# Kernel optimization log

Measured on AMD Instinct MI355X. Metric: run time of the kernel, lower is better.

## Reference

```python
import jax, jax.numpy as jnp
import numpy as np

B, H, S, D = 4, 16, 4096, 64

def _phi(x):
    # feature map for linear attention: elu(x) + 1 (positive features)
    return jax.nn.elu(x) + 1.0

def setup_inputs() -> dict:
    key = jax.random.key(0)
    kq, kk, kv = jax.random.split(key, 3)
    return {
        "query": jax.random.normal(kq, (B, H, S, D), dtype=jnp.float32),
        "key": jax.random.normal(kk, (B, H, S, D), dtype=jnp.float32),
        "value": jax.random.normal(kv, (B, H, S, D), dtype=jnp.float32),
        "attention_mask": jnp.ones((B, S), dtype=jnp.float32),
    }

def reference(query, key, value, attention_mask):
    head_dim = query.shape[-1]
    scale = 1.0 / jnp.sqrt(jnp.sqrt(jnp.float32(head_dim)))
    q = query * scale
    k = key * scale
    phi_q = _phi(q)
    phi_k = _phi(k)
    m = attention_mask[:, None, :, None]  # [B,1,S,1]
    phi_q = phi_q * m
    phi_k = phi_k * m
    # kv_term: [B,H,D,Dv]
    kv_term = jnp.einsum("bhsd,bhse->bhde", phi_k, value)
    out = jnp.einsum("bhsd,bhde->bhse", phi_q, kv_term)
    # normalizer: phi_q @ sum_s phi_k -> [B,H,S,1]
    k_one = jnp.sum(phi_k, axis=-2)  # [B,H,D]
    normalizer = jnp.einsum("bhsd,bhd->bhs", phi_q, k_one)[..., None]
    return out / (normalizer + 1e-8)
```

## Files before the change

### kernel.cpp

```cpp
#include <hip/hip_runtime.h>

#define BDIM 4
#define HDIM 16
#define SDIM 4096
#define DDIM 64
#define NBH (BDIM * HDIM)

#define NC 16
#define BH_STRIDE (DDIM * DDIM + DDIM)
#define CHUNK_FLOATS (NBH * BH_STRIDE)

__device__ __forceinline__ float phi_f(float x) {
    return x > 0.0f ? x + 1.0f : __expf(x);
}

template<bool ATOMIC>
__global__ __launch_bounds__(256, 2) void la_phase1(
    const float* __restrict__ K, const float* __restrict__ V,
    const float* __restrict__ mask, float* __restrict__ outp, int chunk_rows)
{
    __shared__ __align__(16) float smem[8320];

    const int bh = blockIdx.y;
    const int b  = bh / HDIM;
    const int t  = threadIdx.x;
    const int w  = t >> 6;
    const int l  = t & 63;
    const int rowq = l >> 4;
    const int c4   = (l & 15) << 2;
    const int d0   = (l >> 3) << 3;
    const int e0   = (l & 7) << 3;

    float* kT = smem + w * 1024;

    const float* Kb = K + (size_t)bh * SDIM * DDIM;
    const float* Vb = V + (size_t)bh * SDIM * DDIM;
    const float* mb = mask + (size_t)b * SDIM;
    const float scale = 0.35355339059327373f;

    const int rows_per_wave = chunk_rows >> 2;
    const int s_wave = blockIdx.x * chunk_rows + w * rows_per_wave;
    const int ntiles = rows_per_wave >> 4;

    float acc[8][8] = {};
    float k1s[4] = {0.f, 0.f, 0.f, 0.f};

    float4 kr[4]; float mmr[4];
    #pragma unroll
    for (int j = 0; j < 4; ++j) {
        const int s = s_wave + rowq + (j << 2);
        kr[j]  = *(const float4*)(Kb + (size_t)s * DDIM + c4);
        mmr[j] = mb[s];
    }

    for (int tt = 0; tt < ntiles; ++tt) {
        #pragma unroll
        for (int j = 0; j < 4; ++j) {
            float4 p;
            p.x = phi_f(kr[j].x * scale) * mmr[j];
            p.y = phi_f(kr[j].y * scale) * mmr[j];
            p.z = phi_f(kr[j].z * scale) * mmr[j];
            p.w = phi_f(kr[j].w * scale) * mmr[j];
            k1s[0] += p.x; k1s[1] += p.y; k1s[2] += p.z; k1s[3] += p.w;
            *(float4*)&kT[(rowq + (j << 2)) * DDIM + c4] = p;
        }
        if (tt + 1 < ntiles) {
            #pragma unroll
            for (int j = 0; j < 4; ++j) {
                const int s = s_wave + ((tt + 1) << 4) + rowq + (j << 2);
                kr[j]  = *(const float4*)(Kb + (size_t)s * DDIM + c4);
                mmr[j] = mb[s];
            }
        }

        const int s_tile = s_wave + (tt << 4);
        #pragma unroll
        for (int ss = 0; ss < 16; ++ss) {
            const float4 a0 = *(const float4*)&kT[ss * DDIM + d0];
            const float4 a1 = *(const float4*)&kT[ss * DDIM + d0 + 4];
            const float4 v0 = *(const float4*)(Vb + (size_t)(s_tile + ss) * DDIM + e0);
            const float4 v1 = *(const float4*)(Vb + (size_t)(s_tile + ss) * DDIM + e0 + 4);
            const float av[8] = {a0.x, a0.y, a0.z, a0.w, a1.x, a1.y, a1.z, a1.w};
            const float vv[8] = {v0.x, v0.y, v0.z, v0.w, v1.x, v1.y, v1.z, v1.w};
            #pragma unroll
            for (int i = 0; i < 8; ++i)
                #pragma unroll
                for (int j = 0; j < 8; ++j)
                    acc[i][j] += av[i] * vv[j];
        }
    }

    #pragma unroll
    for (int i = 0; i < 4; ++i) {
        k1s[i] += __shfl_xor(k1s[i], 16);
        k1s[i] += __shfl_xor(k1s[i], 32);
    }

    __syncthreads();
    float* bufA = smem;
    float* bufB = smem + 4160;
    if (w < 2) {
        float* Bp = w ? bufB : bufA;
        #pragma unroll
        for (int i = 0; i < 8; ++i) {
            *(float4*)&Bp[(d0 + i) * DDIM + e0]     = make_float4(acc[i][0], acc[i][1], acc[i][2], acc[i][3]);
            *(float4*)&Bp[(d0 + i) * DDIM + e0 + 4] = make_float4(acc[i][4], acc[i][5], acc[i][6], acc[i][7]);
        }
        if (l < 16) *(float4*)&Bp[4096 + (l << 2)] = make_float4(k1s[0], k1s[1], k1s[2], k1s[3]);
    }
    __syncthreads();
    if (w >= 2) {
        float* Bp = (w == 3) ? bufB : bufA;
        #pragma unroll
        for (int i = 0; i < 8; ++i) {
            float4 x0 = *(float4*)&Bp[(d0 + i) * DDIM + e0];
            float4 x1 = *(float4*)&Bp[(d0 + i) * DDIM + e0 + 4];
            x0.x += acc[i][0]; x0.y += acc[i][1]; x0.z += acc[i][2]; x0.w += acc[i][3];
            x1.x += acc[i][4]; x1.y += acc[i][5]; x1.z += acc[i][6]; x1.w += acc[i][7];
            *(float4*)&Bp[(d0 + i) * DDIM + e0]     = x0;
            *(float4*)&Bp[(d0 + i) * DDIM + e0 + 4] = x1;
        }
        if (l < 16) {
            float4 x = *(float4*)&Bp[4096 + (l << 2)];
            x.x += k1s[0]; x.y += k1s[1]; x.z += k1s[2]; x.w += k1s[3];
            *(float4*)&Bp[4096 + (l << 2)] = x;
        }
    }
    __syncthreads();

    float* base = ATOMIC ? (outp + (size_t)bh * BH_STRIDE)
                         : (outp + ((size_t)blockIdx.x * NBH + bh) * BH_STRIDE);
    for (int g = t; g < BH_STRIDE / 4; g += 256) {
        const float4 xa = ((const float4*)bufA)[g];
        const float4 xb = ((const float4*)bufB)[g];
        if (ATOMIC) {
            atomicAdd(&base[4 * g + 0], xa.x + xb.x);
            atomicAdd(&base[4 * g + 1], xa.y + xb.y);
            atomicAdd(&base[4 * g + 2], xa.z + xb.z);
            atomicAdd(&base[4 * g + 3], xa.w + xb.w);
        } else {
            *(float4*)&base[4 * g] = make_float4(xa.x + xb.x, xa.y + xb.y, xa.z + xb.z, xa.w + xb.w);
        }
    }
}

template<int NCT>
__global__ __launch_bounds__(256) void la_reduce(
    const float* __restrict__ part, float* __restrict__ fin)
{
    const int g = blockIdx.x * 256 + threadIdx.x;
    const float4* p4 = (const float4*)part;
    float4 s = p4[g];
    #pragma unroll
    for (int c = 1; c < NCT; ++c) {
        const float4 v = p4[(size_t)c * (CHUNK_FLOATS / 4) + g];
        s.x += v.x; s.y += v.y; s.z += v.z; s.w += v.w;
    }
    ((float4*)fin)[g] = s;
}

__global__ __launch_bounds__(256, 4) void la_phase2(
    const float* __restrict__ Q, const float* __restrict__ mask,
    const float* __restrict__ fin_all, float* __restrict__ out)
{
    __shared__ __align__(16) float kvL[DDIM * DDIM];
    __shared__ __align__(16) float koL[DDIM];
    __shared__ __align__(16) float pqw[4][2][32][4];

    const int bh = blockIdx.y;
    const int b  = bh / HDIM;
    const int t  = threadIdx.x;
    const int w  = t >> 6;
    const int l  = t & 63;
    const int g  = l >> 3;
    const int e0 = (l & 7) << 3;
    const int rbase = blockIdx.x * 128 + (w << 5);
    const int rown  = l & 31;

    const float* fin = fin_all + (size_t)bh * BH_STRIDE;
    {
        const float4* src = (const float4*)fin;
        float4* dst = (float4*)kvL;
        #pragma unroll
        for (int k2 = 0; k2 < 4; ++k2) dst[t + 256 * k2] = src[t + 256 * k2];
        if (t < DDIM) koL[t] = fin[DDIM * DDIM + t];
    }

    const float* Qb   = Q + (size_t)bh * SDIM * DDIM;
    const float* mb   = mask + (size_t)b * SDIM;
    const float* Qrow = Qb + (size_t)(rbase + rown) * DDIM;
    const float scale = 0.35355339059327373f;

    float4 q0 = *(const float4*)(Qrow);
    float4 qn = *(const float4*)(Qrow + 4);
    __syncthreads();

    {
        float4 p;
        p.x = phi_f(q0.x * scale);
        p.y = phi_f(q0.y * scale);
        p.z = phi_f(q0.z * scale);
        p.w = phi_f(q0.w * scale);
        if (l < 32) *(float4*)&pqw[w][0][rown][0] = p;
    }

    float acc[4][8] = {};
    float nrm[4] = {0.f, 0.f, 0.f, 0.f};

    #pragma unroll 1
    for (int dt = 0; dt < 16; ++dt) {
        const int d4  = dt << 2;
        const int cur = dt & 1;
        if (dt < 15) {
            float4 p;
            p.x = phi_f(qn.x * scale);
            p.y = phi_f(qn.y * scale);
            p.z = phi_f(qn.z * scale);
            p.w = phi_f(qn.w * scale);
            if (l < 32) *(float4*)&pqw[w][cur ^ 1][rown][0] = p;
            if (dt < 14) qn = *(const float4*)(Qrow + ((dt + 2) << 2));
        }
        float4 ar[4];
        #pragma unroll
        for (int i = 0; i < 4; ++i)
            ar[i] = *(const float4*)&pqw[w][cur][(g << 2) + i][0];
        const float4 ko4 = *(const float4*)&koL[d4];
        #pragma unroll
        for (int dd = 0; dd < 4; ++dd) {
            const float4 b0 = *(const float4*)&kvL[(d4 + dd) * DDIM + e0];
            const float4 b1 = *(const float4*)&kvL[(d4 + dd) * DDIM + e0 + 4];
            const float kod = (dd == 0) ? ko4.x : (dd == 1) ? ko4.y : (dd == 2) ? ko4.z : ko4.w;
            #pragma unroll
            for (int i = 0; i < 4; ++i) {
                const float a = (dd == 0) ? ar[i].x : (dd == 1) ? ar[i].y : (dd == 2) ? ar[i].z : ar[i].w;
                nrm[i] += a * kod;
                acc[i][0] += a * b0.x; acc[i][1] += a * b0.y; acc[i][2] += a * b0.z; acc[i][3] += a * b0.w;
                acc[i][4] += a * b1.x; acc[i][5] += a * b1.y; acc[i][6] += a * b1.z; acc[i][7] += a * b1.w;
            }
        }
    }

    float* ob = out + (size_t)bh * SDIM * DDIM;
    #pragma unroll
    for (int i = 0; i < 4; ++i) {
        const int r  = rbase + (g << 2) + i;
        const float mm  = mb[r];
        const float inv = mm / (mm * nrm[i] + 1e-8f);
        *(float4*)(ob + (size_t)r * DDIM + e0) =
            make_float4(acc[i][0] * inv, acc[i][1] * inv, acc[i][2] * inv, acc[i][3] * inv);
        *(float4*)(ob + (size_t)r * DDIM + e0 + 4) =
            make_float4(acc[i][4] * inv, acc[i][5] * inv, acc[i][6] * inv, acc[i][7] * inv);
    }
}

extern "C" void kernel_launch(void* const* d_in, const int* in_sizes, int n_in,
                              void* d_out, int out_size, void* d_ws, size_t ws_size,
                              hipStream_t stream) {
    const float* Q = (const float*)d_in[0];
    const float* K = (const float*)d_in[1];
    const float* V = (const float*)d_in[2];
    const float* M = (const float*)d_in[3];
    float* out = (float*)d_out;

    const size_t chunk_bytes = (size_t)CHUNK_FLOATS * sizeof(float);

    if (ws_size >= (size_t)(NC + 1) * chunk_bytes) {
        float* part = (float*)d_ws;
        float* fin  = part + (size_t)NC * CHUNK_FLOATS;
        la_phase1<false><<<dim3(NC, NBH), dim3(256), 0, stream>>>(K, V, M, part, SDIM / NC);
        la_reduce<NC><<<dim3(CHUNK_FLOATS / 4 / 256), dim3(256), 0, stream>>>(part, fin);
        la_phase2<<<dim3(SDIM / 128, NBH), dim3(256), 0, stream>>>(Q, M, fin, out);
    } else {
        float* fin = (float*)d_ws;
        hipMemsetAsync(d_ws, 0, chunk_bytes, stream);
        la_phase1<true><<<dim3(NC, NBH), dim3(256), 0, stream>>>(K, V, M, fin, SDIM / NC);
        la_phase2<<<dim3(SDIM / 128, NBH), dim3(256), 0, stream>>>(Q, M, fin, out);
    }
}
```

Measured before the change: 254.5 us.

## Restructure phase1 to share K tiles across waves with double buffering and more chunks

Phase 1 now has all four waves cooperate on each 16-row K tile. The tile is double-buffered in shared memory. Each wave owns a 16-column slice of the 64x64 output and keeps a 4x4 accumulator instead of 8x8, which removes the cross-wave shared-memory reduction at the end. Register pressure drops, allowing launch bounds of 5 blocks per CU, and the sequence dimension is split into 32 chunks when workspace allows, giving more blocks and parallelism. In exchange there is a __syncthreads per tile, a larger partial buffer and a reduce kernel that reads twice as many partials.

```diff
diff --git a/kernel.cpp b/kernel.cpp
--- a/kernel.cpp
+++ b/kernel.cpp
@@ -6,7 +6,6 @@
 #define DDIM 64
 #define NBH (BDIM * HDIM)
 
-#define NC 16
 #define BH_STRIDE (DDIM * DDIM + DDIM)
 #define CHUNK_FLOATS (NBH * BH_STRIDE)
 
@@ -15,79 +14,107 @@
 }
 
 template<bool ATOMIC>
-__global__ __launch_bounds__(256, 2) void la_phase1(
+__global__ __launch_bounds__(256, 5) void la_phase1(
     const float* __restrict__ K, const float* __restrict__ V,
     const float* __restrict__ mask, float* __restrict__ outp, int chunk_rows)
 {
-    __shared__ __align__(16) float smem[8320];
+    __shared__ __align__(16) float kT[2][16][DDIM];
+    __shared__ __align__(16) float koneP[4][DDIM];
 
     const int bh = blockIdx.y;
     const int b  = bh / HDIM;
     const int t  = threadIdx.x;
     const int w  = t >> 6;
     const int l  = t & 63;
-    const int rowq = l >> 4;
+    const int srow = (w << 2) + (l >> 4);
     const int c4   = (l & 15) << 2;
-    const int d0   = (l >> 3) << 3;
-    const int e0   = (l & 7) << 3;
-
-    float* kT = smem + w * 1024;
+    const int d0   = (l >> 2) << 2;
+    const int e0   = (w << 4) + ((l & 3) << 2);
 
     const float* Kb = K + (size_t)bh * SDIM * DDIM;
     const float* Vb = V + (size_t)bh * SDIM * DDIM;
     const float* mb = mask + (size_t)b * SDIM;
     const float scale = 0.35355339059327373f;
 
-    const int rows_per_wave = chunk_rows >> 2;
-    const int s_wave = blockIdx.x * chunk_rows + w * rows_per_wave;
-    const int ntiles = rows_per_wave >> 4;
-
-    float acc[8][8] = {};
+    const int s_base = blockIdx.x * chunk_rows;
+    const int ntiles = chunk_rows >> 4;
+
+    float acc[4][4] = {};
     float k1s[4] = {0.f, 0.f, 0.f, 0.f};
 
-    float4 kr[4]; float mmr[4];
-    #pragma unroll
-    for (int j = 0; j < 4; ++j) {
-        const int s = s_wave + rowq + (j << 2);
-        kr[j]  = *(const float4*)(Kb + (size_t)s * DDIM + c4);
-        mmr[j] = mb[s];
-    }
+    {
+        const int s = s_base + srow;
+        const float4 kf = *(const float4*)(Kb + (size_t)s * DDIM + c4);
+        const float  m  = mb[s];
+        float4 p;
+        p.x = phi_f(kf.x * scale) * m;
+        p.y = phi_f(kf.y * scale) * m;
+        p.z = phi_f(kf.z * scale) * m;
+        p.w = phi_f(kf.w * scale) * m;
+        k1s[0] += p.x; k1s[1] += p.y; k1s[2] += p.z; k1s[3] += p.w;
+        *(float4*)&kT[0][srow][c4] = p;
+    }
+    __syncthreads();
 
     for (int tt = 0; tt < ntiles; ++tt) {
-        #pragma unroll
-        for (int j = 0; j < 4; ++j) {
+        const int cur = tt & 1;
+        float4 kf; float mnext = 0.f;
+        const bool more = (tt + 1 < ntiles);
+        if (more) {
+            const int s = s_base + ((tt + 1) << 4) + srow;
+            kf = *(const float4*)(Kb + (size_t)s * DDIM + c4);
+            mnext = mb[s];
+        }
+
+        const float* Vt = Vb + (size_t)(s_base + (tt << 4)) * DDIM + e0;
+        float4 vr[8];
+        #pragma unroll
+        for (int ss = 0; ss < 8; ++ss) vr[ss] = *(const float4*)(Vt + (size_t)ss * DDIM);
+        #pragma unroll
+        for (int ss = 0; ss < 8; ++ss) {
+            const float4 a = *(const float4*)&kT[cur][ss][d0];
+            acc[0][0] += a.x * vr[ss].x; acc[0][1] += a.x * vr[ss].y; acc[0][2] += a.x * vr[ss].z; acc[0][3] += a.x * vr[ss].w;
+            acc[1][0] += a.y * vr[ss].x; acc[1][1] += a.y * vr[ss].y; acc[1][2] += a.y * vr[ss].z; acc[1][3] += a.y * vr[ss].w;
+            acc[2][0] += a.z * vr[ss].x; acc[2][1] += a.z * vr[ss].y; acc[2][2] += a.z * vr[ss].z; acc[2][3] += a.z * vr[ss].w;
+            acc[3][0] += a.w * vr[ss].x; acc[3][1] += a.w * vr[ss].y; acc[3][2] += a.w * vr[ss].z; acc[3][3] += a.w * vr[ss].w;
+        }
+        #pragma unroll
+        for (int ss = 0; ss < 8; ++ss) vr[ss] = *(const float4*)(Vt + (size_t)(ss + 8) * DDIM);
+        #pragma unroll
+        for (int ss = 0; ss < 8; ++ss) {
+            const float4 a = *(const float4*)&kT[cur][ss + 8][d0];
+            acc[0][0] += a.x * vr[ss].x; acc[0][1] += a.x * vr[ss].y; acc[0][2] += a.x * vr[ss].z; acc[0][3] += a.x * vr[ss].w;
+            acc[1][0] += a.y * vr[ss].x; acc[1][1] += a.y * vr[ss].y; acc[1][2] += a.y * vr[ss].z; acc[1][3] += a.y * vr[ss].w;
+            acc[2][0] += a.z * vr[ss].x; acc[2][1] += a.z * vr[ss].y; acc[2][2] += a.z * vr[ss].z; acc[2][3] += a.z * vr[ss].w;
+            acc[3][0] += a.w * vr[ss].x; acc[3][1] += a.w * vr[ss].y; acc[3][2] += a.w * vr[ss].z; acc[3][3] += a.w * vr[ss].w;
+        }
+
+        if (more) {
             float4 p;
-            p.x = phi_f(kr[j].x * scale) * mmr[j];
-            p.y = phi_f(kr[j].y * scale) * mmr[j];
-            p.z = phi_f(kr[j].z * scale) * mmr[j];
-            p.w = phi_f(kr[j].w * scale) * mmr[j];
+            p.x = phi_f(kf.x * scale) * mnext;
+            p.y = phi_f(kf.y * scale) * mnext;
+            p.z = phi_f(kf.z * scale) * mnext;
+            p.w = phi_f(kf.w * scale) * mnext;
             k1s[0] += p.x; k1s[1] += p.y; k1s[2] += p.z; k1s[3] += p.w;
-            *(float4*)&kT[(rowq + (j << 2)) * DDIM + c4] = p;
-        }
-        if (tt + 1 < ntiles) {
+            *(float4*)&kT[cur ^ 1][srow][c4] = p;
+        }
+        __syncthreads();
+    }
+
+    float* base = ATOMIC ? (outp + (size_t)bh * BH_STRIDE)
+                         : (outp + ((size_t)blockIdx.x * NBH + bh) * BH_STRIDE);
+
+    if (ATOMIC) {
+        #pragma unroll
+        for (int i = 0; i < 4; ++i)
             #pragma unroll
-            for (int j = 0; j < 4; ++j) {
-                const int s = s_wave + ((tt + 1) << 4) + rowq + (j << 2);
-                kr[j]  = *(const float4*)(Kb + (size_t)s * DDIM + c4);
-                mmr[j] = mb[s];
-            }
-        }
-
-        const int s_tile = s_wave + (tt << 4);
-        #pragma unroll
-        for (int ss = 0; ss < 16; ++ss) {
-            const float4 a0 = *(const float4*)&kT[ss * DDIM + d0];
-            const float4 a1 = *(const float4*)&kT[ss * DDIM + d0 + 4];
-            const float4 v0 = *(const float4*)(Vb + (size_t)(s_tile + ss) * DDIM + e0);
-            const float4 v1 = *(const float4*)(Vb + (size_t)(s_tile + ss) * DDIM + e0 + 4);
-            const float av[8] = {a0.x, a0.y, a0.z, a0.w, a1.x, a1.y, a1.z, a1.w};
-            const float vv[8] = {v0.x, v0.y, v0.z, v0.w, v1.x, v1.y, v1.z, v1.w};
-            #pragma unroll
-            for (int i = 0; i < 8; ++i)
-                #pragma unroll
-                for (int j = 0; j < 8; ++j)
-                    acc[i][j] += av[i] * vv[j];
-        }
+            for (int j = 0; j < 4; ++j)
+                atomicAdd(&base[(d0 + i) * DDIM + e0 + j], acc[i][j]);
+    } else {
+        #pragma unroll
+        for (int i = 0; i < 4; ++i)
+            *(float4*)&base[(d0 + i) * DDIM + e0] =
+                make_float4(acc[i][0], acc[i][1], acc[i][2], acc[i][3]);
     }
 
     #pragma unroll
@@ -95,52 +122,12 @@
         k1s[i] += __shfl_xor(k1s[i], 16);
         k1s[i] += __shfl_xor(k1s[i], 32);
     }
-
+    if (l < 16) *(float4*)&koneP[w][c4] = make_float4(k1s[0], k1s[1], k1s[2], k1s[3]);
     __syncthreads();
-    float* bufA = smem;
-    float* bufB = smem + 4160;
-    if (w < 2) {
-        float* Bp = w ? bufB : bufA;
-        #pragma unroll
-        for (int i = 0; i < 8; ++i) {
-            *(float4*)&Bp[(d0 + i) * DDIM + e0]     = make_float4(acc[i][0], acc[i][1], acc[i][2], acc[i][3]);
-            *(float4*)&Bp[(d0 + i) * DDIM + e0 + 4] = make_float4(acc[i][4], acc[i][5], acc[i][6], acc[i][7]);
-        }
-        if (l < 16) *(float4*)&Bp[4096 + (l << 2)] = make_float4(k1s[0], k1s[1], k1s[2], k1s[3]);
-    }
-    __syncthreads();
-    if (w >= 2) {
-        float* Bp = (w == 3) ? bufB : bufA;
-        #pragma unroll
-        for (int i = 0; i < 8; ++i) {
-            float4 x0 = *(float4*)&Bp[(d0 + i) * DDIM + e0];
-            float4 x1 = *(float4*)&Bp[(d0 + i) * DDIM + e0 + 4];
-            x0.x += acc[i][0]; x0.y += acc[i][1]; x0.z += acc[i][2]; x0.w += acc[i][3];
-            x1.x += acc[i][4]; x1.y += acc[i][5]; x1.z += acc[i][6]; x1.w += acc[i][7];
-            *(float4*)&Bp[(d0 + i) * DDIM + e0]     = x0;
-            *(float4*)&Bp[(d0 + i) * DDIM + e0 + 4] = x1;
-        }
-        if (l < 16) {
-            float4 x = *(float4*)&Bp[4096 + (l << 2)];
-            x.x += k1s[0]; x.y += k1s[1]; x.z += k1s[2]; x.w += k1s[3];
-            *(float4*)&Bp[4096 + (l << 2)] = x;
-        }
-    }
-    __syncthreads();
-
-    float* base = ATOMIC ? (outp + (size_t)bh * BH_STRIDE)
-                         : (outp + ((size_t)blockIdx.x * NBH + bh) * BH_STRIDE);
-    for (int g = t; g < BH_STRIDE / 4; g += 256) {
-        const float4 xa = ((const float4*)bufA)[g];
-        const float4 xb = ((const float4*)bufB)[g];
-        if (ATOMIC) {
-            atomicAdd(&base[4 * g + 0], xa.x + xb.x);
-            atomicAdd(&base[4 * g + 1], xa.y + xb.y);
-            atomicAdd(&base[4 * g + 2], xa.z + xb.z);
-            atomicAdd(&base[4 * g + 3], xa.w + xb.w);
-        } else {
-            *(float4*)&base[4 * g] = make_float4(xa.x + xb.x, xa.y + xb.y, xa.z + xb.z, xa.w + xb.w);
-        }
+    if (t < DDIM) {
+        const float s1 = koneP[0][t] + koneP[1][t] + koneP[2][t] + koneP[3][t];
+        if (ATOMIC) atomicAdd(&base[DDIM * DDIM + t], s1);
+        else        base[DDIM * DDIM + t] = s1;
     }
 }
 
@@ -264,16 +251,22 @@
 
     const size_t chunk_bytes = (size_t)CHUNK_FLOATS * sizeof(float);
 
-    if (ws_size >= (size_t)(NC + 1) * chunk_bytes) {
+    if (ws_size >= 33 * chunk_bytes) {
         float* part = (float*)d_ws;
-        float* fin  = part + (size_t)NC * CHUNK_FLOATS;
-        la_phase1<false><<<dim3(NC, NBH), dim3(256), 0, stream>>>(K, V, M, part, SDIM / NC);
-        la_reduce<NC><<<dim3(CHUNK_FLOATS / 4 / 256), dim3(256), 0, stream>>>(part, fin);
+        float* fin  = part + (size_t)32 * CHUNK_FLOATS;
+        la_phase1<false><<<dim3(32, NBH), dim3(256), 0, stream>>>(K, V, M, part, SDIM / 32);
+        la_reduce<32><<<dim3(CHUNK_FLOATS / 4 / 256), dim3(256), 0, stream>>>(part, fin);
+        la_phase2<<<dim3(SDIM / 128, NBH), dim3(256), 0, stream>>>(Q, M, fin, out);
+    } else if (ws_size >= 17 * chunk_bytes) {
+        float* part = (float*)d_ws;
+        float* fin  = part + (size_t)16 * CHUNK_FLOATS;
+        la_phase1<false><<<dim3(16, NBH), dim3(256), 0, stream>>>(K, V, M, part, SDIM / 16);
+        la_reduce<16><<<dim3(CHUNK_FLOATS / 4 / 256), dim3(256), 0, stream>>>(part, fin);
         la_phase2<<<dim3(SDIM / 128, NBH), dim3(256), 0, stream>>>(Q, M, fin, out);
     } else {
         float* fin = (float*)d_ws;
         hipMemsetAsync(d_ws, 0, chunk_bytes, stream);
-        la_phase1<true><<<dim3(NC, NBH), dim3(256), 0, stream>>>(K, V, M, fin, SDIM / NC);
+        la_phase1<true><<<dim3(16, NBH), dim3(256), 0, stream>>>(K, V, M, fin, SDIM / 16);
         la_phase2<<<dim3(SDIM / 128, NBH), dim3(256), 0, stream>>>(Q, M, fin, out);
     }
 }
```

Measured after the change: 799.8 us. 3.14x slower.

## Stage V through LDS with software pipelining, enlarge phase2 register tile, halve chunks

Applied to the files above, without the earlier changes.

Phase1 now loads K and V tiles into per-wave shared memory and prefetches the next tile in the middle of the current tile's outer-product loop, instead of reading V directly from global memory each step. The k-sum reduction moves to a dedicated LDS slot, and the writeout loop is unrolled. Phase2 gives each thread an 8x8 output tile over 64 rows per wave (256 rows per block) and lays phi(q) out transposed so it can be read as vectors. NC drops from 16 to 8 so there are fewer partial chunks to reduce. The costs are more registers, phase2 occupancy lowered to 2, and fewer phase1 blocks.

```diff
diff --git a/kernel.cpp b/kernel.cpp
--- a/kernel.cpp
+++ b/kernel.cpp
@@ -6,7 +6,7 @@
 #define DDIM 64
 #define NBH (BDIM * HDIM)
 
-#define NC 16
+#define NC 8
 #define BH_STRIDE (DDIM * DDIM + DDIM)
 #define CHUNK_FLOATS (NBH * BH_STRIDE)
 
@@ -19,19 +19,20 @@
     const float* __restrict__ K, const float* __restrict__ V,
     const float* __restrict__ mask, float* __restrict__ outp, int chunk_rows)
 {
-    __shared__ __align__(16) float smem[8320];
+    __shared__ __align__(16) float smem[8576];
 
     const int bh = blockIdx.y;
     const int b  = bh / HDIM;
     const int t  = threadIdx.x;
     const int w  = t >> 6;
     const int l  = t & 63;
-    const int rowq = l >> 4;
-    const int c4   = (l & 15) << 2;
-    const int d0   = (l >> 3) << 3;
-    const int e0   = (l & 7) << 3;
-
-    float* kT = smem + w * 1024;
+    const int rq = l >> 4;
+    const int c4 = (l & 15) << 2;
+    const int d0 = (l >> 3) << 3;
+    const int e0 = (l & 7) << 3;
+
+    float* kS = smem + w * 2048;
+    float* vS = kS + 1024;
 
     const float* Kb = K + (size_t)bh * SDIM * DDIM;
     const float* Vb = V + (size_t)bh * SDIM * DDIM;
@@ -45,49 +46,76 @@
     float acc[8][8] = {};
     float k1s[4] = {0.f, 0.f, 0.f, 0.f};
 
-    float4 kr[4]; float mmr[4];
     #pragma unroll
     for (int j = 0; j < 4; ++j) {
-        const int s = s_wave + rowq + (j << 2);
-        kr[j]  = *(const float4*)(Kb + (size_t)s * DDIM + c4);
-        mmr[j] = mb[s];
-    }
-
+        const int s = s_wave + rq + (j << 2);
+        const float4 kf = *(const float4*)(Kb + (size_t)s * DDIM + c4);
+        const float4 vf = *(const float4*)(Vb + (size_t)s * DDIM + c4);
+        const float  m  = mb[s];
+        float4 p;
+        p.x = phi_f(kf.x * scale) * m;
+        p.y = phi_f(kf.y * scale) * m;
+        p.z = phi_f(kf.z * scale) * m;
+        p.w = phi_f(kf.w * scale) * m;
+        k1s[0] += p.x; k1s[1] += p.y; k1s[2] += p.z; k1s[3] += p.w;
+        *(float4*)&kS[(rq + (j << 2)) * DDIM + c4] = p;
+        *(float4*)&vS[(rq + (j << 2)) * DDIM + c4] = vf;
+    }
+
+    #pragma unroll 1
     for (int tt = 0; tt < ntiles; ++tt) {
         #pragma unroll
-        for (int j = 0; j < 4; ++j) {
-            float4 p;
-            p.x = phi_f(kr[j].x * scale) * mmr[j];
-            p.y = phi_f(kr[j].y * scale) * mmr[j];
-            p.z = phi_f(kr[j].z * scale) * mmr[j];
-            p.w = phi_f(kr[j].w * scale) * mmr[j];
-            k1s[0] += p.x; k1s[1] += p.y; k1s[2] += p.z; k1s[3] += p.w;
-            *(float4*)&kT[(rowq + (j << 2)) * DDIM + c4] = p;
-        }
-        if (tt + 1 < ntiles) {
-            #pragma unroll
-            for (int j = 0; j < 4; ++j) {
-                const int s = s_wave + ((tt + 1) << 4) + rowq + (j << 2);
-                kr[j]  = *(const float4*)(Kb + (size_t)s * DDIM + c4);
-                mmr[j] = mb[s];
-            }
-        }
-
-        const int s_tile = s_wave + (tt << 4);
-        #pragma unroll
-        for (int ss = 0; ss < 16; ++ss) {
-            const float4 a0 = *(const float4*)&kT[ss * DDIM + d0];
-            const float4 a1 = *(const float4*)&kT[ss * DDIM + d0 + 4];
-            const float4 v0 = *(const float4*)(Vb + (size_t)(s_tile + ss) * DDIM + e0);
-            const float4 v1 = *(const float4*)(Vb + (size_t)(s_tile + ss) * DDIM + e0 + 4);
-            const float av[8] = {a0.x, a0.y, a0.z, a0.w, a1.x, a1.y, a1.z, a1.w};
-            const float vv[8] = {v0.x, v0.y, v0.z, v0.w, v1.x, v1.y, v1.z, v1.w};
+        for (int ss = 0; ss < 8; ++ss) {
+            const float4 a0 = *(const float4*)&kS[ss * DDIM + d0];
+            const float4 a1 = *(const float4*)&kS[ss * DDIM + d0 + 4];
+            const float4 v0 = *(const float4*)&vS[ss * DDIM + e0];
+            const float4 v1 = *(const float4*)&vS[ss * DDIM + e0 + 4];
+            const float av[8] = {a0.x,a0.y,a0.z,a0.w,a1.x,a1.y,a1.z,a1.w};
+            const float vv[8] = {v0.x,v0.y,v0.z,v0.w,v1.x,v1.y,v1.z,v1.w};
             #pragma unroll
             for (int i = 0; i < 8; ++i)
                 #pragma unroll
                 for (int j = 0; j < 8; ++j)
                     acc[i][j] += av[i] * vv[j];
         }
+        const bool more = (tt + 1 < ntiles);
+        float4 kf[4], vf[4]; float mm4[4];
+        if (more) {
+            #pragma unroll
+            for (int j = 0; j < 4; ++j) {
+                const int s = s_wave + ((tt + 1) << 4) + rq + (j << 2);
+                kf[j]  = *(const float4*)(Kb + (size_t)s * DDIM + c4);
+                vf[j]  = *(const float4*)(Vb + (size_t)s * DDIM + c4);
+                mm4[j] = mb[s];
+            }
+        }
+        #pragma unroll
+        for (int ss = 8; ss < 16; ++ss) {
+            const float4 a0 = *(const float4*)&kS[ss * DDIM + d0];
+            const float4 a1 = *(const float4*)&kS[ss * DDIM + d0 + 4];
+            const float4 v0 = *(const float4*)&vS[ss * DDIM + e0];
+            const float4 v1 = *(const float4*)&vS[ss * DDIM + e0 + 4];
+            const float av[8] = {a0.x,a0.y,a0.z,a0.w,a1.x,a1.y,a1.z,a1.w};
+            const float vv[8] = {v0.x,v0.y,v0.z,v0.w,v1.x,v1.y,v1.z,v1.w};
+            #pragma unroll
+            for (int i = 0; i < 8; ++i)
+                #pragma unroll
+                for (int j = 0; j < 8; ++j)
+                    acc[i][j] += av[i] * vv[j];
+        }
+        if (more) {
+            #pragma unroll
+            for (int j = 0; j < 4; ++j) {
+                float4 p;
+                p.x = phi_f(kf[j].x * scale) * mm4[j];
+                p.y = phi_f(kf[j].y * scale) * mm4[j];
+                p.z = phi_f(kf[j].z * scale) * mm4[j];
+                p.w = phi_f(kf[j].w * scale) * mm4[j];
+                k1s[0] += p.x; k1s[1] += p.y; k1s[2] += p.z; k1s[3] += p.w;
+                *(float4*)&kS[(rq + (j << 2)) * DDIM + c4] = p;
+                *(float4*)&vS[(rq + (j << 2)) * DDIM + c4] = vf[j];
+            }
+        }
     }
 
     #pragma unroll
@@ -99,6 +127,8 @@
     __syncthreads();
     float* bufA = smem;
     float* bufB = smem + 4160;
+    float* koP  = smem + 8320;
+    if (l < 16) *(float4*)&koP[(w << 6) + c4] = make_float4(k1s[0], k1s[1], k1s[2], k1s[3]);
     if (w < 2) {
         float* Bp = w ? bufB : bufA;
         #pragma unroll
@@ -106,7 +136,6 @@
             *(float4*)&Bp[(d0 + i) * DDIM + e0]     = make_float4(acc[i][0], acc[i][1], acc[i][2], acc[i][3]);
             *(float4*)&Bp[(d0 + i) * DDIM + e0 + 4] = make_float4(acc[i][4], acc[i][5], acc[i][6], acc[i][7]);
         }
-        if (l < 16) *(float4*)&Bp[4096 + (l << 2)] = make_float4(k1s[0], k1s[1], k1s[2], k1s[3]);
     }
     __syncthreads();
     if (w >= 2) {
@@ -120,27 +149,29 @@
             *(float4*)&Bp[(d0 + i) * DDIM + e0]     = x0;
             *(float4*)&Bp[(d0 + i) * DDIM + e0 + 4] = x1;
         }
-        if (l < 16) {
-            float4 x = *(float4*)&Bp[4096 + (l << 2)];
-            x.x += k1s[0]; x.y += k1s[1]; x.z += k1s[2]; x.w += k1s[3];
-            *(float4*)&Bp[4096 + (l << 2)] = x;
-        }
     }
     __syncthreads();
 
     float* base = ATOMIC ? (outp + (size_t)bh * BH_STRIDE)
                          : (outp + ((size_t)blockIdx.x * NBH + bh) * BH_STRIDE);
-    for (int g = t; g < BH_STRIDE / 4; g += 256) {
+    #pragma unroll
+    for (int k2 = 0; k2 < 4; ++k2) {
+        const int g = t + 256 * k2;
         const float4 xa = ((const float4*)bufA)[g];
         const float4 xb = ((const float4*)bufB)[g];
         if (ATOMIC) {
-            atomicAdd(&base[4 * g + 0], xa.x + xb.x);
-            atomicAdd(&base[4 * g + 1], xa.y + xb.y);
-            atomicAdd(&base[4 * g + 2], xa.z + xb.z);
-            atomicAdd(&base[4 * g + 3], xa.w + xb.w);
+            atomicAdd(&base[4*g + 0], xa.x + xb.x);
+            atomicAdd(&base[4*g + 1], xa.y + xb.y);
+            atomicAdd(&base[4*g + 2], xa.z + xb.z);
+            atomicAdd(&base[4*g + 3], xa.w + xb.w);
         } else {
-            *(float4*)&base[4 * g] = make_float4(xa.x + xb.x, xa.y + xb.y, xa.z + xb.z, xa.w + xb.w);
-        }
+            *(float4*)&base[4*g] = make_float4(xa.x + xb.x, xa.y + xb.y, xa.z + xb.z, xa.w + xb.w);
+        }
+    }
+    if (t < DDIM) {
+        const float s1 = koP[t] + koP[64 + t] + koP[128 + t] + koP[192 + t];
+        if (ATOMIC) atomicAdd(&base[DDIM * DDIM + t], s1);
+        else        base[DDIM * DDIM + t] = s1;
     }
 }
 
@@ -159,23 +190,22 @@
     ((float4*)fin)[g] = s;
 }
 
-__global__ __launch_bounds__(256, 4) void la_phase2(
+__global__ __launch_bounds__(256, 2) void la_phase2(
     const float* __restrict__ Q, const float* __restrict__ mask,
     const float* __restrict__ fin_all, float* __restrict__ out)
 {
     __shared__ __align__(16) float kvL[DDIM * DDIM];
     __shared__ __align__(16) float koL[DDIM];
-    __shared__ __align__(16) float pqw[4][2][32][4];
+    __shared__ __align__(16) float pq[4][2][4][64];
 
     const int bh = blockIdx.y;
     const int b  = bh / HDIM;
     const int t  = threadIdx.x;
     const int w  = t >> 6;
     const int l  = t & 63;
-    const int g  = l >> 3;
+    const int rg = l >> 3;
     const int e0 = (l & 7) << 3;
-    const int rbase = blockIdx.x * 128 + (w << 5);
-    const int rown  = l & 31;
+    const int rbase = blockIdx.x * 256 + (w << 6);
 
     const float* fin = fin_all + (size_t)bh * BH_STRIDE;
     {
@@ -188,7 +218,7 @@
 
     const float* Qb   = Q + (size_t)bh * SDIM * DDIM;
     const float* mb   = mask + (size_t)b * SDIM;
-    const float* Qrow = Qb + (size_t)(rbase + rown) * DDIM;
+    const float* Qrow = Qb + (size_t)(rbase + l) * DDIM;
     const float scale = 0.35355339059327373f;
 
     float4 q0 = *(const float4*)(Qrow);
@@ -196,54 +226,50 @@
     __syncthreads();
 
     {
-        float4 p;
-        p.x = phi_f(q0.x * scale);
-        p.y = phi_f(q0.y * scale);
-        p.z = phi_f(q0.z * scale);
-        p.w = phi_f(q0.w * scale);
-        if (l < 32) *(float4*)&pqw[w][0][rown][0] = p;
-    }
-
-    float acc[4][8] = {};
-    float nrm[4] = {0.f, 0.f, 0.f, 0.f};
+        pq[w][0][0][l] = phi_f(q0.x * scale);
+        pq[w][0][1][l] = phi_f(q0.y * scale);
+        pq[w][0][2][l] = phi_f(q0.z * scale);
+        pq[w][0][3][l] = phi_f(q0.w * scale);
+    }
+
+    float acc[8][8] = {};
+    float nrm[8] = {0.f,0.f,0.f,0.f,0.f,0.f,0.f,0.f};
 
     #pragma unroll 1
     for (int dt = 0; dt < 16; ++dt) {
         const int d4  = dt << 2;
         const int cur = dt & 1;
         if (dt < 15) {
-            float4 p;
-            p.x = phi_f(qn.x * scale);
-            p.y = phi_f(qn.y * scale);
-            p.z = phi_f(qn.z * scale);
-            p.w = phi_f(qn.w * scale);
-            if (l < 32) *(float4*)&pqw[w][cur ^ 1][rown][0] = p;
+            pq[w][cur ^ 1][0][l] = phi_f(qn.x * scale);
+            pq[w][cur ^ 1][1][l] = phi_f(qn.y * scale);
+            pq[w][cur ^ 1][2][l] = phi_f(qn.z * scale);
+            pq[w][cur ^ 1][3][l] = phi_f(qn.w * scale);
             if (dt < 14) qn = *(const float4*)(Qrow + ((dt + 2) << 2));
         }
-        float4 ar[4];
-        #pragma unroll
-        for (int i = 0; i < 4; ++i)
-            ar[i] = *(const float4*)&pqw[w][cur][(g << 2) + i][0];
         const float4 ko4 = *(const float4*)&koL[d4];
         #pragma unroll
         for (int dd = 0; dd < 4; ++dd) {
-            const float4 b0 = *(const float4*)&kvL[(d4 + dd) * DDIM + e0];
-            const float4 b1 = *(const float4*)&kvL[(d4 + dd) * DDIM + e0 + 4];
+            const float4 af0 = *(const float4*)&pq[w][cur][dd][rg << 3];
+            const float4 af1 = *(const float4*)&pq[w][cur][dd][(rg << 3) + 4];
+            const float4 b0  = *(const float4*)&kvL[(d4 + dd) * DDIM + e0];
+            const float4 b1  = *(const float4*)&kvL[(d4 + dd) * DDIM + e0 + 4];
             const float kod = (dd == 0) ? ko4.x : (dd == 1) ? ko4.y : (dd == 2) ? ko4.z : ko4.w;
-            #pragma unroll
-            for (int i = 0; i < 4; ++i) {
-                const float a = (dd == 0) ? ar[i].x : (dd == 1) ? ar[i].y : (dd == 2) ? ar[i].z : ar[i].w;
-                nrm[i] += a * kod;
-                acc[i][0] += a * b0.x; acc[i][1] += a * b0.y; acc[i][2] += a * b0.z; acc[i][3] += a * b0.w;
-                acc[i][4] += a * b1.x; acc[i][5] += a * b1.y; acc[i][6] += a * b1.z; acc[i][7] += a * b1.w;
+            const float av[8] = {af0.x,af0.y,af0.z,af0.w,af1.x,af1.y,af1.z,af1.w};
+            const float bv[8] = {b0.x,b0.y,b0.z,b0.w,b1.x,b1.y,b1.z,b1.w};
+            #pragma unroll
+            for (int i = 0; i < 8; ++i) {
+                nrm[i] += av[i] * kod;
+                #pragma unroll
+                for (int j = 0; j < 8; ++j)
+                    acc[i][j] += av[i] * bv[j];
             }
         }
     }
 
     float* ob = out + (size_t)bh * SDIM * DDIM;
     #pragma unroll
-    for (int i = 0; i < 4; ++i) {
-        const int r  = rbase + (g << 2) + i;
+    for (int i = 0; i < 8; ++i) {
+        const int r  = rbase + (rg << 3) + i;
         const float mm  = mb[r];
         const float inv = mm / (mm * nrm[i] + 1e-8f);
         *(float4*)(ob + (size_t)r * DDIM + e0) =
@@ -269,11 +295,11 @@
         float* fin  = part + (size_t)NC * CHUNK_FLOATS;
         la_phase1<false><<<dim3(NC, NBH), dim3(256), 0, stream>>>(K, V, M, part, SDIM / NC);
         la_reduce<NC><<<dim3(CHUNK_FLOATS / 4 / 256), dim3(256), 0, stream>>>(part, fin);
-        la_phase2<<<dim3(SDIM / 128, NBH), dim3(256), 0, stream>>>(Q, M, fin, out);
+        la_phase2<<<dim3(SDIM / 256, NBH), dim3(256), 0, stream>>>(Q, M, fin, out);
     } else {
         float* fin = (float*)d_ws;
         hipMemsetAsync(d_ws, 0, chunk_bytes, stream);
         la_phase1<true><<<dim3(NC, NBH), dim3(256), 0, stream>>>(K, V, M, fin, SDIM / NC);
-        la_phase2<<<dim3(SDIM / 128, NBH), dim3(256), 0, stream>>>(Q, M, fin, out);
-    }
-}
+        la_phase2<<<dim3(SDIM / 256, NBH), dim3(256), 0, stream>>>(Q, M, fin, out);
+    }
+}
```

New measurement: 449.3 us. 1.77x slower.
